# Kernel tuning notes

Measured on AMD Instinct MI355X. Metric: run time of the kernel, lower is better.

Reference implementation:

```python
import jax, jax.numpy as jnp
import numpy as np

N = 50000      # nodes
E = 800000     # edges (avg degree 16)
D_IN = 64
H = 128        # capacity
LAT = 64       # latent_dim
LN_EPS = 1e-5


def setup_inputs() -> dict:
    key = jax.random.key(0)
    ks = jax.random.split(key, 16)
    inp = {}
    inp["x"] = jax.random.normal(ks[0], (N, D_IN), dtype=jnp.float32)
    inp["edge_index"] = jax.random.randint(ks[1], (2, E), 0, N)
    dims = [(D_IN, H), (H, H), (H, LAT)]
    ki = 2
    for t in ("m", "v"):  # mu tower / logvar tower
        for i, (di, do) in enumerate(dims):
            s = 1.0 / np.sqrt(di)
            inp[f"{t}Wl{i}"] = jax.random.normal(ks[ki], (do, di), jnp.float32) * s; ki += 1
            inp[f"{t}bl{i}"] = jnp.zeros((do,), jnp.float32)
            inp[f"{t}Wr{i}"] = jax.random.normal(ks[ki], (do, di), jnp.float32) * s; ki += 1
            if i < 2:  # LayerNorm on hidden layers only
                inp[f"{t}g{i}"] = jnp.ones((do,), jnp.float32)
                inp[f"{t}b{i}"] = jnp.zeros((do,), jnp.float32)
    return inp


def _ln(h, g, b):
    m = h.mean(-1, keepdims=True)
    v = h.var(-1, keepdims=True)
    return (h - m) * jax.lax.rsqrt(v + LN_EPS) * g + b


def _sage(h, src, dst, inv_deg, Wl, bl, Wr):
    # mean neighbor aggregation: scatter-add messages h[src] into dst, divide by degree
    agg = jax.ops.segment_sum(h[src], dst, num_segments=N) * inv_deg  # [N, d_in]
    # PyG SAGEConv: lin_l(agg) [with bias] + lin_r(h_root) [no bias]
    return agg @ Wl.T + bl + h @ Wr.T


def _tower(x, src, dst, inv_deg, layers):
    h = x
    L = len(layers)
    for i, lay in enumerate(layers):
        h = _sage(h, src, dst, inv_deg, lay[0], lay[1], lay[2])
        if i < L - 1:
            h = jax.nn.relu(_ln(h, lay[3], lay[4]))
    return h


def reference(x, edge_index,
              mWl0, mbl0, mWr0, mg0, mb0,
              mWl1, mbl1, mWr1, mg1, mb1,
              mWl2, mbl2, mWr2,
              vWl0, vbl0, vWr0, vg0, vb0,
              vWl1, vbl1, vWr1, vg1, vb1,
              vWl2, vbl2, vWr2):
    src, dst = edge_index[0], edge_index[1]
    deg = jax.ops.segment_sum(jnp.ones((E,), x.dtype), dst, num_segments=N)
    inv_deg = (1.0 / jnp.maximum(deg, 1.0))[:, None]
    mu_layers = [(mWl0, mbl0, mWr0, mg0, mb0),
                 (mWl1, mbl1, mWr1, mg1, mb1),
                 (mWl2, mbl2, mWr2)]
    lv_layers = [(vWl0, vbl0, vWr0, vg0, vb0),
                 (vWl1, vbl1, vWr1, vg1, vb1),
                 (vWl2, vbl2, vWr2)]
    mu = _tower(x, src, dst, inv_deg, mu_layers)
    lv = _tower(x, src, dst, inv_deg, lv_layers)
    return mu, lv
```

## Files before the change

kernel.cpp:

```cpp
#include <hip/hip_runtime.h>

#define NN 50000
#define NE 800000
#define MPAD 50048
#define NBK 196
#define FB 98
#define CH4 2048
#define EB4 200000
#define STAGE_CAP 6144

typedef __attribute__((ext_vector_type(8))) short short8;
typedef __attribute__((ext_vector_type(4))) float f32x4;
typedef uint __attribute__((ext_vector_type(4))) uintx4;
typedef uint __attribute__((ext_vector_type(2))) uintx2;

__device__ __forceinline__ ushort f2b(float f) {
    uint u = __builtin_bit_cast(uint, f);
    uint r = (u + 0x7fffu + ((u >> 16) & 1u)) >> 16;
    return (ushort)r;
}
__device__ __forceinline__ uint pk2(float a, float b) {
    return (uint)f2b(a) | ((uint)f2b(b) << 16);
}
__device__ __forceinline__ float blo(uint u) { return __builtin_bit_cast(float, u << 16); }
__device__ __forceinline__ float bhi(uint u) { return __builtin_bit_cast(float, u & 0xffff0000u); }

__device__ __forceinline__ uint enc8u(float y) {
    uint b = __builtin_bit_cast(uint, y * 0x1p-120f) + (1u << 19);
    return (b >> 20) & 0x7fu;
}
__device__ __forceinline__ uint enc8s(float y) {
    uint sb = __builtin_bit_cast(uint, y) & 0x80000000u;
    uint b = __builtin_bit_cast(uint, fabsf(y) * 0x1p-120f) + (1u << 19);
    return ((b >> 20) & 0x7fu) | (sb >> 24);
}

__device__ __forceinline__ void acc4(float* a, uintx2 u) {
    a[0] += blo(u[0]); a[1] += bhi(u[0]);
    a[2] += blo(u[1]); a[3] += bhi(u[1]);
}
template <bool SIGNED>
__device__ __forceinline__ void accf8(float* a, uintx2 u, float c120) {
#pragma unroll
    for (int w = 0; w < 2; ++w) {
        uint v = u[w];
#pragma unroll
        for (int j = 0; j < 4; ++j) {
            uint b = (v >> (8 * j)) & 0xffu;
            uint f = SIGNED ? (((b & 0x80u) << 24) | ((b & 0x7fu) << 20)) : (b << 20);
            a[w * 4 + j] += __builtin_bit_cast(float, f) * c120;
        }
    }
}


struct W2Args {
    const float* srcA[8];
    const float* srcB[8];
    ushort* dst[8];
};


struct PrepArgs {
    const float* x; ushort* xb;
    W2Args w;
    const int* edst; int* bhist;
};

__global__ __launch_bounds__(256) void k_prep(PrepArgs a) {
    __shared__ int h[NBK];
    int b = blockIdx.x;
    int t = threadIdx.x;
    if (b < FB) {
        for (int i = t; i < NBK; i += 256) h[i] = 0;
        __syncthreads();
        int i1 = min((b + 1) * CH4, EB4);
        for (int i = b * CH4 + t; i < i1; i += 256) {
            int4 d = ((const int4*)a.edst)[i];
            atomicAdd(&h[d.x >> 8], 1);
            atomicAdd(&h[d.y >> 8], 1);
            atomicAdd(&h[d.z >> 8], 1);
            atomicAdd(&h[d.w >> 8], 1);
        }
        __syncthreads();
        for (int i = t; i < NBK; i += 256) a.bhist[b * NBK + i] = h[i];
    } else if (b < FB + 512) {
        const int offT[8]   = {0, 16384, 49152, 57344, 65536, 81920, 114688, 122880};
        const int splitT[8] = {64, 128, 128, 0, 64, 128, 128, 0};
        const int logKKT[8] = {7, 8, 7, 7, 7, 8, 7, 7};
        const int ntT[8]    = {8, 8, 4, 4, 8, 8, 4, 4};
        int idx = (b - FB) * 256 + t;
        if (idx >= 131072) return;
        int L = 0;
#pragma unroll
        for (int i = 1; i < 8; ++i) if (idx >= offT[i]) L = i;
        int j = idx - offT[L];
        int lk = logKKT[L];
        int KK = 1 << lk;
        int n = j >> lk;
        int c = j & (KK - 1);
        int split = splitT[L];
        float v = (c < split) ? a.w.srcA[L][n * split + c]
                              : a.w.srcB[L][n * (KK - split) + (c - split)];
        int ks = c >> 5, kseg = (c >> 3) & 3, jj = c & 7;
        int nt = n >> 4, r15 = n & 15;
        int lane = (kseg << 4) | r15;
        int foff = ((ks * ntT[L] + nt) << 9) + (lane << 3) + jj;
        a.w.dst[L][foff] = f2b(v);
    } else {
        int i = (b - FB - 512) * 256 + t;
        if (i < NN * 32) {
            float2 v = *(const float2*)(a.x + (size_t)i * 2);
            *(uint*)(a.xb + (size_t)i * 2) = pk2(v.x, v.y);
        }
    }
}


__global__ __launch_bounds__(256) void k_fscan(const int* __restrict__ bhist,
                                               int* __restrict__ pairRel,
                                               int* __restrict__ bbase) {
    __shared__ int tot[256];
    int b = threadIdx.x;
    int run = 0;
    if (b < NBK) {
        for (int blk = 0; blk < FB; ++blk) {
            int v = bhist[blk * NBK + b];
            pairRel[blk * NBK + b] = run;
            run += v;
        }
    }
    tot[b] = (b < NBK) ? run : 0;
    __syncthreads();
    for (int off = 1; off < 256; off <<= 1) {
        int t = (b >= off) ? tot[b - off] : 0;
        __syncthreads();
        tot[b] += t;
        __syncthreads();
    }
    if (b < NBK) bbase[b] = tot[b] - run;
    if (b == NBK - 1) bbase[NBK] = tot[b];
}

__global__ __launch_bounds__(256) void k_f2(const int* __restrict__ src, const int* __restrict__ dst,
                                            const int* __restrict__ pairRel,
                                            const int* __restrict__ bbase, int2* __restrict__ pairs) {
    __shared__ int cur[NBK];
    for (int i = threadIdx.x; i < NBK; i += 256)
        cur[i] = bbase[i] + pairRel[blockIdx.x * NBK + i];
    __syncthreads();
    int i1 = min((int)(blockIdx.x + 1) * CH4, EB4);
    for (int i = blockIdx.x * CH4 + threadIdx.x; i < i1; i += 256) {
        int4 s = ((const int4*)src)[i];
        int4 d = ((const int4*)dst)[i];
        int p0 = atomicAdd(&cur[d.x >> 8], 1);
        int p1 = atomicAdd(&cur[d.y >> 8], 1);
        int p2 = atomicAdd(&cur[d.z >> 8], 1);
        int p3 = atomicAdd(&cur[d.w >> 8], 1);
        pairs[p0] = (int2){s.x, d.x};
        pairs[p1] = (int2){s.y, d.y};
        pairs[p2] = (int2){s.z, d.z};
        pairs[p3] = (int2){s.w, d.w};
    }
}

__global__ __launch_bounds__(256) void k_f3(const int2* __restrict__ pairs,
                                            const int* __restrict__ bbase,
                                            int* __restrict__ row_start,
                                            float* __restrict__ inv_deg,
                                            int* __restrict__ col) {
    __shared__ int ndeg[256];
    __shared__ int noff[256];
    __shared__ int stage[STAGE_CAP];
    int b = blockIdx.x;
    int base = bbase[b], end = bbase[b + 1];
    int nbase = b << 8;
    int t = threadIdx.x;
    ndeg[t] = 0;
    __syncthreads();
    for (int p = base + t; p < end; p += 256) atomicAdd(&ndeg[pairs[p].y - nbase], 1);
    __syncthreads();
    int d = ndeg[t];
    noff[t] = d;
    __syncthreads();
    for (int off = 1; off < 256; off <<= 1) {
        int v = (t >= off) ? noff[t - off] : 0;
        __syncthreads();
        noff[t] += v;
        __syncthreads();
    }
    int excl = noff[t] - d;
    int node = nbase + t;
    if (node < NN) {
        row_start[node] = base + excl;
        inv_deg[node] = 1.0f / (float)(d > 1 ? d : 1);
    }
    if (b == 0 && t == 0) row_start[NN] = NE;
    __syncthreads();
    noff[t] = excl;
    __syncthreads();
    int cnt = end - base;
    for (int p = base + t; p < end; p += 256) {
        int2 pr = pairs[p];
        int pos = atomicAdd(&noff[pr.y - nbase], 1);
        if (pos < STAGE_CAP) stage[pos] = pr.x;
        else col[base + pos] = pr.x;
    }
    __syncthreads();
    int lim = cnt < STAGE_CAP ? cnt : STAGE_CAP;
    for (int i = t; i < lim; i += 256) col[base + i] = stage[i];
}


__global__ __launch_bounds__(256) void k_agg64(
    const ushort* __restrict__ h,
    const int* __restrict__ row_start, const int* __restrict__ col,
    const float* __restrict__ inv_deg, ushort* __restrict__ o) {
    int gid = blockIdx.x * 256 + threadIdx.x;
    int node = gid >> 4;
    int li = gid & 15;
    if (node >= NN) return;
    int s = row_start[node], e = row_start[node + 1];
    float sc = inv_deg[node];
    const ushort* hb = h + li * 4;
    float a[4] = {0, 0, 0, 0};
    int p = s;
    for (; p + 7 < e; p += 8) {
        int cc[8];
#pragma unroll
        for (int j = 0; j < 8; ++j) cc[j] = __builtin_nontemporal_load(col + p + j);
#pragma unroll
        for (int j = 0; j < 8; ++j) acc4(a, *(const uintx2*)(hb + (size_t)cc[j] * 64));
    }
    for (; p < e; ++p) acc4(a, *(const uintx2*)(hb + (size_t)col[p] * 64));
    uintx2 r;
    r[0] = pk2(a[0] * sc, a[1] * sc);
    r[1] = pk2(a[2] * sc, a[3] * sc);
    *(uintx2*)(o + (size_t)node * 64 + li * 4) = r;
}


template <int D, bool SIGNED>
__global__ __launch_bounds__(256) void k_agg8(
    const uchar* __restrict__ h,
    const int* __restrict__ row_start, const int* __restrict__ col,
    const float* __restrict__ inv_deg, ushort* __restrict__ o) {
    constexpr int LPN = D / 8;
    int gid = blockIdx.x * 256 + threadIdx.x;
    int node = gid / LPN;
    int li = gid & (LPN - 1);
    if (node >= NN) return;
    int s = row_start[node], e = row_start[node + 1];
    float sc = inv_deg[node];
    const uchar* hb = h + li * 8;
    const float c120 = 0x1p120f;
    float a[8] = {0, 0, 0, 0, 0, 0, 0, 0};
    int p = s;
    for (; p + 7 < e; p += 8) {
        int cc[8];
#pragma unroll
        for (int j = 0; j < 8; ++j) cc[j] = __builtin_nontemporal_load(col + p + j);
#pragma unroll
        for (int j = 0; j < 8; ++j) accf8<SIGNED>(a, *(const uintx2*)(hb + (size_t)cc[j] * D), c120);
    }
    for (; p < e; ++p) accf8<SIGNED>(a, *(const uintx2*)(hb + (size_t)col[p] * D), c120);
    uintx4 r;
    r[0] = pk2(a[0] * sc, a[1] * sc);
    r[1] = pk2(a[2] * sc, a[3] * sc);
    r[2] = pk2(a[4] * sc, a[5] * sc);
    r[3] = pk2(a[6] * sc, a[7] * sc);
    *(uintx4*)(o + (size_t)node * D + li * 8) = r;
}


struct GArgs {
    const ushort *A1, *A2, *Wm, *Wv;
    const float *blm, *blv, *gm, *gv, *bbm, *bbv;
    void* out;
    uchar* out8;
};

template <int KH, int NOUT, bool DO_LN, bool DUAL, int ASTR, int AOFFM, int OSTR, int OOFFM, bool F8OUT, int RT>
__global__ __launch_bounds__(256, 3) void k_gemm(GArgs a) {
    constexpr int NT = NOUT / 16;
    constexpr int NK = KH / 16;
    constexpr int TW = DUAL ? 2 : 1;
    constexpr int KSB = (TW * NT >= 16) ? 1 : (16 / (TW * NT));
    constexpr int NC = NK / KSB;
    constexpr int TCH = KSB * NT * 64;
    constexpr int CPT = TW * TCH;
    __shared__ uint4 wlds[2][CPT];

    int tid = threadIdx.x;
    int lane = tid & 63, wid = tid >> 6;
    int tow = DUAL ? 0 : blockIdx.y;
    int aoff = tow * AOFFM;
    const uint4* w0g = (const uint4*)(tow ? a.Wv : a.Wm);
    const uint4* w1g = (const uint4*)a.Wv;

    int r15 = lane & 15, kseg = lane >> 4;
    int m0 = blockIdx.x * (64 * RT) + wid * (16 * RT);
    size_t ar[RT];
#pragma unroll
    for (int t = 0; t < RT; ++t) ar[t] = (size_t)(m0 + t * 16 + r15);

    short8 af[2][RT][KSB];

    auto stageW = [&](int c, int b) {
        const uint4* p0 = w0g + (size_t)c * TCH;
#pragma unroll
        for (int i = 0; i < TCH / 256; ++i) wlds[b][i * 256 + tid] = p0[i * 256 + tid];
        if (DUAL) {
            const uint4* p1 = w1g + (size_t)c * TCH;
#pragma unroll
            for (int i = 0; i < TCH / 256; ++i) wlds[b][TCH + i * 256 + tid] = p1[i * 256 + tid];
        }
    };
    auto loadA = [&](int c, int b) {
#pragma unroll
        for (int ko = 0; ko < KSB; ++ko) {
            int kc = (c * KSB + ko) * 32 + kseg * 8;
#pragma unroll
            for (int t = 0; t < RT; ++t)
                af[b][t][ko] = (kc < KH) ? *(const short8*)(a.A1 + ar[t] * ASTR + aoff + kc)
                                         : *(const short8*)(a.A2 + ar[t] * ASTR + aoff + (kc - KH));
        }
    };

    loadA(0, 0);
    stageW(0, 0);
    __syncthreads();

    f32x4 acc[TW][RT][NT];
#pragma unroll
    for (int tt = 0; tt < TW; ++tt)
#pragma unroll
        for (int t = 0; t < RT; ++t)
#pragma unroll
            for (int nt = 0; nt < NT; ++nt) acc[tt][t][nt] = (f32x4){0.f, 0.f, 0.f, 0.f};

#pragma unroll
    for (int c = 0; c < NC; ++c) {
        int b = c & 1;
        if (c + 1 < NC) { stageW(c + 1, b ^ 1); loadA(c + 1, b ^ 1); }
#pragma unroll
        for (int ko = 0; ko < KSB; ++ko) {
#pragma unroll
            for (int nt = 0; nt < NT; ++nt) {
#pragma unroll
                for (int tt = 0; tt < TW; ++tt) {
                    short8 w = *(const short8*)&wlds[b][tt * TCH + (ko * NT + nt) * 64 + lane];
#pragma unroll
                    for (int t = 0; t < RT; ++t)
                        acc[tt][t][nt] = __builtin_amdgcn_mfma_f32_16x16x32_bf16(af[b][t][ko], w, acc[tt][t][nt], 0, 0, 0);
                }
            }
        }
        __syncthreads();
    }

#pragma unroll
    for (int tt = 0; tt < TW; ++tt) {
        int tsel = DUAL ? tt : tow;
        int ooff = tsel * OOFFM;
        const float* bl = tsel ? a.blv : a.blm;
#pragma unroll
        for (int nt = 0; nt < NT; ++nt) {
            float bb = bl[nt * 16 + r15];
#pragma unroll
            for (int t = 0; t < RT; ++t)
#pragma unroll
                for (int r = 0; r < 4; ++r) acc[tt][t][nt][r] += bb;
        }
        if (DO_LN) {
            const float* g = tsel ? a.gv : a.gm;
            const float* b2 = tsel ? a.bbv : a.bbm;
#pragma unroll
            for (int t = 0; t < RT; ++t) {
                float s[4] = {0, 0, 0, 0}, q[4] = {0, 0, 0, 0};
#pragma unroll
                for (int nt = 0; nt < NT; ++nt)
#pragma unroll
                    for (int r = 0; r < 4; ++r) { float v = acc[tt][t][nt][r]; s[r] += v; q[r] += v * v; }
#pragma unroll
                for (int off = 1; off < 16; off <<= 1)
#pragma unroll
                    for (int r = 0; r < 4; ++r) { s[r] += __shfl_xor(s[r], off); q[r] += __shfl_xor(q[r], off); }
                float mean[4], rstd[4];
#pragma unroll
                for (int r = 0; r < 4; ++r) {
                    mean[r] = s[r] * (1.0f / NOUT);
                    float var = q[r] * (1.0f / NOUT) - mean[r] * mean[r];
                    rstd[r] = rsqrtf(var + 1e-5f);
                }
                ushort* out = (ushort*)a.out;
#pragma unroll
                for (int nt = 0; nt < NT; ++nt) {
                    int n = nt * 16 + r15;
                    float gg = g[n], bb = b2[n];
#pragma unroll
                    for (int r = 0; r < 4; ++r) {
                        int row = m0 + t * 16 + kseg * 4 + r;
                        if (row < NN) {
                            float y = fmaxf((acc[tt][t][nt][r] - mean[r]) * rstd[r] * gg + bb, 0.0f);
                            out[(size_t)row * OSTR + ooff + n] = f2b(y);
                            if (F8OUT) a.out8[(size_t)row * OSTR + ooff + n] = (uchar)enc8u(y);
                        }
                    }
                }
            }
        } else {
            float* out = (float*)a.out;
#pragma unroll
            for (int t = 0; t < RT; ++t)
#pragma unroll
                for (int nt = 0; nt < NT; ++nt) {
                    int n = nt * 16 + r15;
#pragma unroll
                    for (int r = 0; r < 4; ++r) {
                        int row = m0 + t * 16 + kseg * 4 + r;
                        if (row < NN) out[(size_t)row * OSTR + ooff + n] = acc[tt][t][nt][r];
                    }
                }
        }
    }
}


struct G2Args {
    const ushort *A, *Wm, *Wv, *a2;
    const float *blm, *blv;
    void *outm, *outv;
};

template <bool FINAL>
__global__ __launch_bounds__(256, 2) void k_gemm2(G2Args a) {
    constexpr int NT = 4, NK = 4;
    constexpr int WCH = 1024;
    __shared__ uint4 wlds[WCH];

    int tid = threadIdx.x;
    int lane = tid & 63, wid = tid >> 6;
    int tow = blockIdx.y;
    {
        const uint4* w0 = (const uint4*)(tow ? a.Wv : a.Wm);
        for (int i = tid; i < WCH; i += 256) wlds[i] = w0[i];
    }
    int r15 = lane & 15, kseg = lane >> 4;
    int m0 = blockIdx.x * 128 + wid * 32;
    size_t ar0 = (size_t)(m0 + r15);
    size_t ar1 = (size_t)(m0 + 16 + r15);
    int aoff = tow * 128;

    short8 af[2][NK];
#pragma unroll
    for (int ks = 0; ks < NK; ++ks) {
        int kc = ks * 32 + kseg * 8;
        af[0][ks] = *(const short8*)(a.A + ar0 * 256 + aoff + kc);
        af[1][ks] = *(const short8*)(a.A + ar1 * 256 + aoff + kc);
    }
    __syncthreads();

    f32x4 acc[2][NT];
#pragma unroll
    for (int t = 0; t < 2; ++t)
#pragma unroll
        for (int nt = 0; nt < NT; ++nt) acc[t][nt] = (f32x4){0.f, 0.f, 0.f, 0.f};

#pragma unroll
    for (int ks = 0; ks < NK; ++ks) {
#pragma unroll
        for (int nt = 0; nt < NT; ++nt) {
            short8 w = *(const short8*)&wlds[(ks * NT + nt) * 64 + lane];
            acc[0][nt] = __builtin_amdgcn_mfma_f32_16x16x32_bf16(af[0][ks], w, acc[0][nt], 0, 0, 0);
            acc[1][nt] = __builtin_amdgcn_mfma_f32_16x16x32_bf16(af[1][ks], w, acc[1][nt], 0, 0, 0);
        }
    }

    if (FINAL) {
        const float* bl = tow ? a.blv : a.blm;
        float* out = (float*)(tow ? a.outv : a.outm);
#pragma unroll
        for (int t = 0; t < 2; ++t)
#pragma unroll
            for (int nt = 0; nt < NT; ++nt) {
                int n = nt * 16 + r15;
                float bb = bl[n];
#pragma unroll
                for (int r = 0; r < 4; ++r) {
                    int row = m0 + t * 16 + kseg * 4 + r;
                    if (row < NN) {
                        float av = blo((uint)a.a2[(size_t)row * 128 + tow * 64 + n]);
                        out[(size_t)row * 64 + n] = acc[t][nt][r] + bb + av;
                    }
                }
            }
    } else {
        uchar* out = (uchar*)a.outm;
#pragma unroll
        for (int t = 0; t < 2; ++t)
#pragma unroll
            for (int nt = 0; nt < NT; ++nt) {
                int n = nt * 16 + r15;
#pragma unroll
                for (int r = 0; r < 4; ++r) {
                    int row = m0 + t * 16 + kseg * 4 + r;
                    if (row < NN) out[(size_t)row * 128 + tow * 64 + n] = (uchar)enc8s(acc[t][nt][r]);
                }
            }
    }
}


extern "C" void kernel_launch(void* const* d_in, const int* in_sizes, int n_in,
                              void* d_out, int out_size, void* d_ws, size_t ws_size,
                              hipStream_t stream) {
    const float* x = (const float*)d_in[0];
    const int* ei = (const int*)d_in[1];
    const int* esrc = ei;
    const int* edst = ei + NE;

    const float* mWl0 = (const float*)d_in[2];
    const float* mbl0 = (const float*)d_in[3];
    const float* mWr0 = (const float*)d_in[4];
    const float* mg0  = (const float*)d_in[5];
    const float* mb0  = (const float*)d_in[6];
    const float* mWl1 = (const float*)d_in[7];
    const float* mbl1 = (const float*)d_in[8];
    const float* mWr1 = (const float*)d_in[9];
    const float* mg1  = (const float*)d_in[10];
    const float* mb1  = (const float*)d_in[11];
    const float* mWl2 = (const float*)d_in[12];
    const float* mbl2 = (const float*)d_in[13];
    const float* mWr2 = (const float*)d_in[14];
    const float* vWl0 = (const float*)d_in[15];
    const float* vbl0 = (const float*)d_in[16];
    const float* vWr0 = (const float*)d_in[17];
    const float* vg0  = (const float*)d_in[18];
    const float* vb0  = (const float*)d_in[19];
    const float* vWl1 = (const float*)d_in[20];
    const float* vbl1 = (const float*)d_in[21];
    const float* vWr1 = (const float*)d_in[22];
    const float* vg1  = (const float*)d_in[23];
    const float* vb1  = (const float*)d_in[24];
    const float* vWl2 = (const float*)d_in[25];
    const float* vbl2 = (const float*)d_in[26];
    const float* vWr2 = (const float*)d_in[27];

    char* p = (char*)d_ws;
    auto alloc = [&](size_t bytes) {
        void* r = (void*)p;
        p += (bytes + 255) & ~(size_t)255;
        return r;
    };
    int* bhist     = (int*)alloc((size_t)FB * NBK * 4);
    int* pairRel   = (int*)alloc((size_t)FB * NBK * 4);
    int* bbase     = (int*)alloc((size_t)(NBK + 1) * 4);
    int* row_start = (int*)alloc((size_t)(NN + 1) * 4);
    float* inv_deg = (float*)alloc((size_t)NN * 4);
    int* col       = (int*)alloc((size_t)NE * 4);
    int2* pairs    = (int2*)alloc((size_t)NE * 8);
    ushort* agg0   = (ushort*)pairs;
    ushort* x_bf   = (ushort*)alloc((size_t)MPAD * 64 * 2);
    ushort* h1p    = (ushort*)alloc((size_t)MPAD * 256 * 2);
    ushort* h2p    = (ushort*)alloc((size_t)MPAD * 256 * 2);
    ushort* aggp   = (ushort*)alloc((size_t)MPAD * 256 * 2);
    uchar* h1f8    = (uchar*)h2p;
    uchar* p2f8    = (uchar*)aggp;
    ushort* a2     = aggp + (size_t)MPAD * 128;
    ushort* wc0    = (ushort*)alloc((size_t)128 * 128 * 2);
    ushort* wc1    = (ushort*)alloc((size_t)128 * 256 * 2);
    ushort* wc2    = (ushort*)alloc((size_t)64 * 128 * 2);
    ushort* wc3    = (ushort*)alloc((size_t)128 * 128 * 2);
    ushort* wc4    = (ushort*)alloc((size_t)128 * 256 * 2);
    ushort* wc5    = (ushort*)alloc((size_t)64 * 128 * 2);
    ushort* wc6    = (ushort*)alloc((size_t)64 * 128 * 2);
    ushort* wc7    = (ushort*)alloc((size_t)64 * 128 * 2);

    float* out_mu = (float*)d_out;
    float* out_lv = (float*)d_out + (size_t)NN * 64;

    PrepArgs pa;
    pa.x = x; pa.xb = x_bf; pa.edst = edst; pa.bhist = bhist;
    pa.w.srcA[0] = mWl0; pa.w.srcB[0] = mWr0; pa.w.dst[0] = wc0;
    pa.w.srcA[1] = mWl1; pa.w.srcB[1] = mWr1; pa.w.dst[1] = wc1;
    pa.w.srcA[2] = mWl2; pa.w.srcB[2] = nullptr; pa.w.dst[2] = wc2;
    pa.w.srcA[3] = nullptr; pa.w.srcB[3] = mWr2; pa.w.dst[3] = wc6;
    pa.w.srcA[4] = vWl0; pa.w.srcB[4] = vWr0; pa.w.dst[4] = wc3;
    pa.w.srcA[5] = vWl1; pa.w.srcB[5] = vWr1; pa.w.dst[5] = wc4;
    pa.w.srcA[6] = vWl2; pa.w.srcB[6] = nullptr; pa.w.dst[6] = wc5;
    pa.w.srcA[7] = nullptr; pa.w.srcB[7] = vWr2; pa.w.dst[7] = wc7;
    k_prep<<<FB + 512 + (NN * 32 + 255) / 256, 256, 0, stream>>>(pa);

    k_fscan<<<1, 256, 0, stream>>>(bhist, pairRel, bbase);
    k_f2<<<FB, 256, 0, stream>>>(esrc, edst, pairRel, bbase, pairs);
    k_f3<<<NBK, 256, 0, stream>>>(pairs, bbase, row_start, inv_deg, col);

    k_agg64<<<(NN * 16 + 255) / 256, 256, 0, stream>>>(x_bf, row_start, col, inv_deg, agg0);
    {
        GArgs ga = {agg0, x_bf, wc0, wc3, mbl0, vbl0, mg0, vg0, mb0, vb0, h1p, h1f8};
        k_gemm<64, 128, true, true, 64, 0, 256, 128, true, 1><<<dim3(MPAD / 64, 1), 256, 0, stream>>>(ga);
    }
    k_agg8<256, false><<<(NN * 32 + 255) / 256, 256, 0, stream>>>(h1f8, row_start, col, inv_deg, aggp);
    {
        GArgs ga = {aggp, h1p, wc1, wc4, mbl1, vbl1, mg1, vg1, mb1, vb1, h2p, nullptr};
        k_gemm<128, 128, true, false, 256, 128, 256, 128, false, 2><<<dim3(MPAD / 128, 2), 256, 0, stream>>>(ga);
    }
    {
        G2Args g2 = {h2p, wc2, wc5, nullptr, nullptr, nullptr, p2f8, nullptr};
        k_gemm2<false><<<dim3(MPAD / 128, 2), 256, 0, stream>>>(g2);
    }
    k_agg8<128, true><<<(NN * 16 + 255) / 256, 256, 0, stream>>>(p2f8, row_start, col, inv_deg, a2);
    {
        G2Args g2 = {h2p, wc6, wc7, a2, mbl2, vbl2, out_mu, out_lv};
        k_gemm2<true><<<dim3(MPAD / 128, 2), 256, 0, stream>>>(g2);
    }
}
```

Baseline: 329.3 us.

## Fuse layer-2 projection into layer-1 GEMM epilogue and widen aggregation loads

The layer-1 GEMM now writes its post-LayerNorm bf16 tile to shared memory and runs the Wl2 projection in the same kernel, producing the fp8 projected features directly. This removes the separate k_gemm2<false> launch and its re-read of h2 from global memory. The aggregation kernels also use 16-byte loads per lane with half as many lanes per node, giving fewer, wider gathers. The cost is more registers per thread and a larger shared-memory footprint in the fused GEMM, which may lower occupancy.

```diff
diff --git a/kernel.cpp b/kernel.cpp
--- a/kernel.cpp
+++ b/kernel.cpp
@@ -35,14 +35,14 @@
     return ((b >> 20) & 0x7fu) | (sb >> 24);
 }
 
-__device__ __forceinline__ void acc4(float* a, uintx2 u) {
-    a[0] += blo(u[0]); a[1] += bhi(u[0]);
-    a[2] += blo(u[1]); a[3] += bhi(u[1]);
+__device__ __forceinline__ void accb16(float* a, uintx4 u) {
+#pragma unroll
+    for (int w = 0; w < 4; ++w) { a[2 * w] += blo(u[w]); a[2 * w + 1] += bhi(u[w]); }
 }
 template <bool SIGNED>
-__device__ __forceinline__ void accf8(float* a, uintx2 u, float c120) {
-#pragma unroll
-    for (int w = 0; w < 2; ++w) {
+__device__ __forceinline__ void accf8x4(float* a, uintx4 u, float c120) {
+#pragma unroll
+    for (int w = 0; w < 4; ++w) {
         uint v = u[w];
 #pragma unroll
         for (int j = 0; j < 4; ++j) {
@@ -217,26 +217,26 @@
     const int* __restrict__ row_start, const int* __restrict__ col,
     const float* __restrict__ inv_deg, ushort* __restrict__ o) {
     int gid = blockIdx.x * 256 + threadIdx.x;
-    int node = gid >> 4;
-    int li = gid & 15;
+    int node = gid >> 3;
+    int li = gid & 7;
     if (node >= NN) return;
     int s = row_start[node], e = row_start[node + 1];
     float sc = inv_deg[node];
-    const ushort* hb = h + li * 4;
-    float a[4] = {0, 0, 0, 0};
+    const ushort* hb = h + li * 8;
+    float a[8] = {0, 0, 0, 0, 0, 0, 0, 0};
     int p = s;
     for (; p + 7 < e; p += 8) {
         int cc[8];
 #pragma unroll
         for (int j = 0; j < 8; ++j) cc[j] = __builtin_nontemporal_load(col + p + j);
 #pragma unroll
-        for (int j = 0; j < 8; ++j) acc4(a, *(const uintx2*)(hb + (size_t)cc[j] * 64));
-    }
-    for (; p < e; ++p) acc4(a, *(const uintx2*)(hb + (size_t)col[p] * 64));
-    uintx2 r;
-    r[0] = pk2(a[0] * sc, a[1] * sc);
-    r[1] = pk2(a[2] * sc, a[3] * sc);
-    *(uintx2*)(o + (size_t)node * 64 + li * 4) = r;
+        for (int j = 0; j < 8; ++j) accb16(a, *(const uintx4*)(hb + (size_t)cc[j] * 64));
+    }
+    for (; p < e; ++p) accb16(a, *(const uintx4*)(hb + (size_t)col[p] * 64));
+    uintx4 r;
+#pragma unroll
+    for (int w = 0; w < 4; ++w) r[w] = pk2(a[2 * w] * sc, a[2 * w + 1] * sc);
+    *(uintx4*)(o + (size_t)node * 64 + li * 8) = r;
 }
 
 
@@ -245,31 +245,35 @@
     const uchar* __restrict__ h,
     const int* __restrict__ row_start, const int* __restrict__ col,
     const float* __restrict__ inv_deg, ushort* __restrict__ o) {
-    constexpr int LPN = D / 8;
+    constexpr int LPN = D / 16;
     int gid = blockIdx.x * 256 + threadIdx.x;
     int node = gid / LPN;
     int li = gid & (LPN - 1);
     if (node >= NN) return;
     int s = row_start[node], e = row_start[node + 1];
     float sc = inv_deg[node];
-    const uchar* hb = h + li * 8;
+    const uchar* hb = h + li * 16;
     const float c120 = 0x1p120f;
-    float a[8] = {0, 0, 0, 0, 0, 0, 0, 0};
+    float a[16];
+#pragma unroll
+    for (int i = 0; i < 16; ++i) a[i] = 0.f;
     int p = s;
     for (; p + 7 < e; p += 8) {
         int cc[8];
 #pragma unroll
         for (int j = 0; j < 8; ++j) cc[j] = __builtin_nontemporal_load(col + p + j);
 #pragma unroll
-        for (int j = 0; j < 8; ++j) accf8<SIGNED>(a, *(const uintx2*)(hb + (size_t)cc[j] * D), c120);
-    }
-    for (; p < e; ++p) accf8<SIGNED>(a, *(const uintx2*)(hb + (size_t)col[p] * D), c120);
-    uintx4 r;
-    r[0] = pk2(a[0] * sc, a[1] * sc);
-    r[1] = pk2(a[2] * sc, a[3] * sc);
-    r[2] = pk2(a[4] * sc, a[5] * sc);
-    r[3] = pk2(a[6] * sc, a[7] * sc);
-    *(uintx4*)(o + (size_t)node * D + li * 8) = r;
+        for (int j = 0; j < 8; ++j) accf8x4<SIGNED>(a, *(const uintx4*)(hb + (size_t)cc[j] * D), c120);
+    }
+    for (; p < e; ++p) accf8x4<SIGNED>(a, *(const uintx4*)(hb + (size_t)col[p] * D), c120);
+    uintx4 r0, r1;
+#pragma unroll
+    for (int w = 0; w < 4; ++w) {
+        r0[w] = pk2(a[2 * w] * sc, a[2 * w + 1] * sc);
+        r1[w] = pk2(a[8 + 2 * w] * sc, a[8 + 2 * w + 1] * sc);
+    }
+    *(uintx4*)(o + (size_t)node * D + li * 16) = r0;
+    *(uintx4*)(o + (size_t)node * D + li * 16 + 8) = r1;
 }
 
 
@@ -278,9 +282,12 @@
     const float *blm, *blv, *gm, *gv, *bbm, *bbv;
     void* out;
     uchar* out8;
+    const ushort *Wpm, *Wpv;
+    uchar* pout;
 };
 
-template <int KH, int NOUT, bool DO_LN, bool DUAL, int ASTR, int AOFFM, int OSTR, int OOFFM, bool F8OUT, int RT>
+template <int KH, int NOUT, bool DO_LN, bool DUAL, int ASTR, int AOFFM, int OSTR, int OOFFM,
+          bool F8OUT, int RT, bool PROJ>
 __global__ __launch_bounds__(256, 3) void k_gemm(GArgs a) {
     constexpr int NT = NOUT / 16;
     constexpr int NK = KH / 16;
@@ -289,7 +296,11 @@
     constexpr int NC = NK / KSB;
     constexpr int TCH = KSB * NT * 64;
     constexpr int CPT = TW * TCH;
-    __shared__ uint4 wlds[2][CPT];
+    constexpr int PADL = 136;
+    constexpr int SMEM = PROJ ? (128 * PADL * 2) : (2 * CPT * 16);
+    __shared__ char smem[SMEM];
+    uint4* wlds = (uint4*)smem;
+    ushort* h2s = (ushort*)smem;
 
     int tid = threadIdx.x;
     int lane = tid & 63, wid = tid >> 6;
@@ -300,6 +311,7 @@
 
     int r15 = lane & 15, kseg = lane >> 4;
     int m0 = blockIdx.x * (64 * RT) + wid * (16 * RT);
+    int lrb = wid * (16 * RT);
     size_t ar[RT];
 #pragma unroll
     for (int t = 0; t < RT; ++t) ar[t] = (size_t)(m0 + t * 16 + r15);
@@ -309,11 +321,11 @@
     auto stageW = [&](int c, int b) {
         const uint4* p0 = w0g + (size_t)c * TCH;
 #pragma unroll
-        for (int i = 0; i < TCH / 256; ++i) wlds[b][i * 256 + tid] = p0[i * 256 + tid];
+        for (int i = 0; i < TCH / 256; ++i) wlds[b * CPT + i * 256 + tid] = p0[i * 256 + tid];
         if (DUAL) {
             const uint4* p1 = w1g + (size_t)c * TCH;
 #pragma unroll
-            for (int i = 0; i < TCH / 256; ++i) wlds[b][TCH + i * 256 + tid] = p1[i * 256 + tid];
+            for (int i = 0; i < TCH / 256; ++i) wlds[b * CPT + TCH + i * 256 + tid] = p1[i * 256 + tid];
         }
     };
     auto loadA = [&](int c, int b) {
@@ -349,7 +361,7 @@
             for (int nt = 0; nt < NT; ++nt) {
 #pragma unroll
                 for (int tt = 0; tt < TW; ++tt) {
-                    short8 w = *(const short8*)&wlds[b][tt * TCH + (ko * NT + nt) * 64 + lane];
+                    short8 w = *(const short8*)&wlds[b * CPT + tt * TCH + (ko * NT + nt) * 64 + lane];
 #pragma unroll
                     for (int t = 0; t < RT; ++t)
                         acc[tt][t][nt] = __builtin_amdgcn_mfma_f32_16x16x32_bf16(af[b][t][ko], w, acc[tt][t][nt], 0, 0, 0);
@@ -401,9 +413,11 @@
 #pragma unroll
                     for (int r = 0; r < 4; ++r) {
                         int row = m0 + t * 16 + kseg * 4 + r;
+                        float y = fmaxf((acc[tt][t][nt][r] - mean[r]) * rstd[r] * gg + bb, 0.0f);
+                        ushort yb = f2b(y);
+                        if (PROJ) h2s[(lrb + t * 16 + kseg * 4 + r) * PADL + n] = yb;
                         if (row < NN) {
-                            float y = fmaxf((acc[tt][t][nt][r] - mean[r]) * rstd[r] * gg + bb, 0.0f);
-                            out[(size_t)row * OSTR + ooff + n] = f2b(y);
+                            out[(size_t)row * OSTR + ooff + n] = yb;
                             if (F8OUT) a.out8[(size_t)row * OSTR + ooff + n] = (uchar)enc8u(y);
                         }
                     }
@@ -424,6 +438,40 @@
                 }
         }
     }
+
+    if (PROJ) {
+        const ushort* wp = tow ? a.Wpv : a.Wpm;
+        f32x4 acc2[RT][4];
+#pragma unroll
+        for (int t = 0; t < RT; ++t)
+#pragma unroll
+            for (int nt = 0; nt < 4; ++nt) acc2[t][nt] = (f32x4){0.f, 0.f, 0.f, 0.f};
+#pragma unroll
+        for (int ks = 0; ks < 4; ++ks) {
+            short8 afr[RT];
+#pragma unroll
+            for (int t = 0; t < RT; ++t)
+                afr[t] = *(const short8*)&h2s[(lrb + t * 16 + r15) * PADL + ks * 32 + kseg * 8];
+#pragma unroll
+            for (int nt = 0; nt < 4; ++nt) {
+                short8 w = *(const short8*)(wp + (size_t)((ks * 4 + nt) * 64 + lane) * 8);
+#pragma unroll
+                for (int t = 0; t < RT; ++t)
+                    acc2[t][nt] = __builtin_amdgcn_mfma_f32_16x16x32_bf16(afr[t], w, acc2[t][nt], 0, 0, 0);
+            }
+        }
+#pragma unroll
+        for (int t = 0; t < RT; ++t)
+#pragma unroll
+            for (int nt = 0; nt < 4; ++nt) {
+                int n = nt * 16 + r15;
+#pragma unroll
+                for (int r = 0; r < 4; ++r) {
+                    int row = m0 + t * 16 + kseg * 4 + r;
+                    if (row < NN) a.pout[(size_t)row * 128 + tow * 64 + n] = (uchar)enc8s(acc2[t][nt][r]);
+                }
+            }
+    }
 }
 
 
@@ -433,8 +481,7 @@
     void *outm, *outv;
 };
 
-template <bool FINAL>
-__global__ __launch_bounds__(256, 2) void k_gemm2(G2Args a) {
+__global__ __launch_bounds__(256, 2) void k_gemm2f(G2Args a) {
     constexpr int NT = 4, NK = 4;
     constexpr int WCH = 1024;
     __shared__ uint4 wlds[WCH];
@@ -477,38 +524,23 @@
         }
     }
 
-    if (FINAL) {
-        const float* bl = tow ? a.blv : a.blm;
-        float* out = (float*)(tow ? a.outv : a.outm);
-#pragma unroll
-        for (int t = 0; t < 2; ++t)
-#pragma unroll
-            for (int nt = 0; nt < NT; ++nt) {
-                int n = nt * 16 + r15;
-                float bb = bl[n];
-#pragma unroll
-                for (int r = 0; r < 4; ++r) {
-                    int row = m0 + t * 16 + kseg * 4 + r;
-                    if (row < NN) {
-                        float av = blo((uint)a.a2[(size_t)row * 128 + tow * 64 + n]);
-                        out[(size_t)row * 64 + n] = acc[t][nt][r] + bb + av;
-                    }
+    const float* bl = tow ? a.blv : a.blm;
+    float* out = (float*)(tow ? a.outv : a.outm);
+#pragma unroll
+    for (int t = 0; t < 2; ++t)
+#pragma unroll
+        for (int nt = 0; nt < NT; ++nt) {
+            int n = nt * 16 + r15;
+            float bb = bl[n];
+#pragma unroll
+            for (int r = 0; r < 4; ++r) {
+                int row = m0 + t * 16 + kseg * 4 + r;
+                if (row < NN) {
+                    float av = blo((uint)a.a2[(size_t)row * 128 + tow * 64 + n]);
+                    out[(size_t)row * 64 + n] = acc[t][nt][r] + bb + av;
                 }
             }
-    } else {
-        uchar* out = (uchar*)a.outm;
-#pragma unroll
-        for (int t = 0; t < 2; ++t)
-#pragma unroll
-            for (int nt = 0; nt < NT; ++nt) {
-                int n = nt * 16 + r15;
-#pragma unroll
-                for (int r = 0; r < 4; ++r) {
-                    int row = m0 + t * 16 + kseg * 4 + r;
-                    if (row < NN) out[(size_t)row * 128 + tow * 64 + n] = (uchar)enc8s(acc[t][nt][r]);
-                }
-            }
-    }
+        }
 }
 
 
@@ -596,23 +628,23 @@
     k_f2<<<FB, 256, 0, stream>>>(esrc, edst, pairRel, bbase, pairs);
     k_f3<<<NBK, 256, 0, stream>>>(pairs, bbase, row_start, inv_deg, col);
 
-    k_agg64<<<(NN * 16 + 255) / 256, 256, 0, stream>>>(x_bf, row_start, col, inv_deg, agg0);
+    k_agg64<<<(NN * 8 + 255) / 256, 256, 0, stream>>>(x_bf, row_start, col, inv_deg, agg0);
     {
-        GArgs ga = {agg0, x_bf, wc0, wc3, mbl0, vbl0, mg0, vg0, mb0, vb0, h1p, h1f8};
-        k_gemm<64, 128, true, true, 64, 0, 256, 128, true, 1><<<dim3(MPAD / 64, 1), 256, 0, stream>>>(ga);
-    }
-    k_agg8<256, false><<<(NN * 32 + 255) / 256, 256, 0, stream>>>(h1f8, row_start, col, inv_deg, aggp);
+        GArgs ga = {agg0, x_bf, wc0, wc3, mbl0, vbl0, mg0, vg0, mb0, vb0, h1p, h1f8,
+                    nullptr, nullptr, nullptr};
+        k_gemm<64, 128, true, true, 64, 0, 256, 128, true, 1, false>
+            <<<dim3(MPAD / 64, 1), 256, 0, stream>>>(ga);
+    }
+    k_agg8<256, false><<<(NN * 16 + 255) / 256, 256, 0, stream>>>(h1f8, row_start, col, inv_deg, aggp);
     {
-        GArgs ga = {aggp, h1p, wc1, wc4, mbl1, vbl1, mg1, vg1, mb1, vb1, h2p, nullptr};
-        k_gemm<128, 128, true, false, 256, 128, 256, 128, false, 2><<<dim3(MPAD / 128, 2), 256, 0, stream>>>(ga);
-    }
-    {
-        G2Args g2 = {h2p, wc2, wc5, nullptr, nullptr, nullptr, p2f8, nullptr};
-        k_gemm2<false><<<dim3(MPAD / 128, 2), 256, 0, stream>>>(g2);
-    }
-    k_agg8<128, true><<<(NN * 16 + 255) / 256, 256, 0, stream>>>(p2f8, row_start, col, inv_deg, a2);
+        GArgs ga = {aggp, h1p, wc1, wc4, mbl1, vbl1, mg1, vg1, mb1, vb1, h2p, nullptr,
+                    wc2, wc5, p2f8};
+        k_gemm<128, 128, true, false, 256, 128, 256, 128, false, 2, true>
+            <<<dim3(MPAD / 128, 2), 256, 0, stream>>>(ga);
+    }
+    k_agg8<128, true><<<(NN * 8 + 255) / 256, 256, 0, stream>>>(p2f8, row_start, col, inv_deg, a2);
     {
         G2Args g2 = {h2p, wc6, wc7, a2, mbl2, vbl2, out_mu, out_lv};
-        k_gemm2<true><<<dim3(MPAD / 128, 2), 256, 0, stream>>>(g2);
-    }
-}
+        k_gemm2f<<<dim3(MPAD / 128, 2), 256, 0, stream>>>(g2);
+    }
+}
```

After: 373.5 us. 1.13x slower.
